# Optimization experiments

Hardware: AMD Instinct MI355X
Metric: run time of the kernel (lower is better)

The kernel has to match this reference:

```python
import jax, jax.numpy as jnp
import numpy as np

N = 65536
APP = 1024
SP = 512
HID = 512
CARD = 16
SUB = HID // CARD  # 32


def setup_inputs() -> dict:
    key = jax.random.key(0)
    ks = jax.random.split(key, 8)
    s1 = 1.0 / np.sqrt(APP)
    s2 = 1.0 / np.sqrt(SP)
    s3 = 1.0 / np.sqrt(SUB)
    return {
        "appearance": jax.random.normal(ks[0], (N, APP), jnp.float32),
        "spatial": jax.random.normal(ks[1], (N, SP), jnp.float32),
        # Batched per-branch weights (torch Linear: y = x @ W.T + b; here stored as [in, out])
        "W1": jax.random.uniform(ks[2], (CARD, APP, SUB), jnp.float32, -s1, s1),
        "b1": jax.random.uniform(ks[3], (CARD, SUB), jnp.float32, -s1, s1),
        "W2": jax.random.uniform(ks[4], (CARD, SP, SUB), jnp.float32, -s2, s2),
        "b2": jax.random.uniform(ks[5], (CARD, SP if False else SUB), jnp.float32, -s2, s2),
        "W3": jax.random.uniform(ks[6], (CARD, SUB, HID), jnp.float32, -s3, s3),
        "b3": jax.random.uniform(ks[7], (CARD, HID), jnp.float32, -s3, s3),
    }


def reference(appearance, spatial, W1, b1, W2, b2, W3, b3):
    # fc1[c] = appearance @ W1[c] + b1[c]; fc2[c] = spatial @ W2[c] + b2[c]
    h1 = jnp.einsum('na,cas->ncs', appearance, W1) + b1[None]  # [N, C, SUB]
    h2 = jnp.einsum('np,cps->ncs', spatial, W2) + b2[None]     # [N, C, SUB]
    h = jax.nn.relu(h1 + h2)
    # sum over branches of (h[:,c] @ W3[c] + b3[c]) == einsum + sum of biases
    out = jnp.einsum('ncs,csh->nh', h, W3) + jnp.sum(b3, axis=0)[None]  # [N, HID]
    return jax.nn.relu(out)
```

## Files before the change

kernel.cpp:

```cpp
#include <hip/hip_runtime.h>
#include <hip/hip_bf16.h>

typedef __attribute__((ext_vector_type(4))) float floatx4;
typedef __attribute__((ext_vector_type(8))) short bf16x8;

__device__ __forceinline__ unsigned short f2bf(float f) {
    union { float f; unsigned u; } v; v.f = f;
    unsigned r = v.u + 0x7fffu + ((v.u >> 16) & 1u);
    return (unsigned short)(r >> 16);
}

__device__ __forceinline__ bf16x8 cvt8(float4 lo, float4 hi) {
    union { __hip_bfloat16 b[8]; bf16x8 v; } u;
    u.b[0] = __float2bfloat16(lo.x); u.b[1] = __float2bfloat16(lo.y);
    u.b[2] = __float2bfloat16(lo.z); u.b[3] = __float2bfloat16(lo.w);
    u.b[4] = __float2bfloat16(hi.x); u.b[5] = __float2bfloat16(hi.y);
    u.b[6] = __float2bfloat16(hi.z); u.b[7] = __float2bfloat16(hi.w);
    return u.v;
}

__device__ __forceinline__ void dma16(const void* gsrc, void* ldst) {
    __builtin_amdgcn_global_load_lds(
        (const __attribute__((address_space(1))) unsigned*)gsrc,
        (__attribute__((address_space(3))) unsigned*)ldst, 16, 0, 0);
}

__global__ void prep_kernel(const float* __restrict__ W1, const float* __restrict__ b1,
                            const float* __restrict__ W2, const float* __restrict__ b2,
                            const float* __restrict__ W3, const float* __restrict__ b3,
                            unsigned short* __restrict__ wcat, unsigned short* __restrict__ w3f,
                            float* __restrict__ bias12, float* __restrict__ bias3s)
{
    int tid = blockIdx.x * 256 + threadIdx.x;
    if (tid < 98304) {
        int l  = tid & 63;
        int nt = (tid >> 6) & 31;
        int kc = tid >> 11;
        int n  = nt * 16 + (l & 15);
        int k0 = kc * 32 + ((l >> 4) << 3);
        int c = n >> 5, s = n & 31;
        union { unsigned short us[8]; int4 v; } pk;
        const float* src = (k0 < 1024) ? (W1 + c * 32768 + k0 * 32 + s)
                                       : (W2 + c * 16384 + (k0 - 1024) * 32 + s);
        #pragma unroll
        for (int j = 0; j < 8; ++j) pk.us[j] = f2bf(src[j * 32]);
        *(int4*)(wcat + (size_t)tid * 8) = pk.v;
    } else if (tid < 131072) {
        int t  = tid - 98304;
        int l  = t & 63;
        int nt = (t >> 6) & 31;
        int kc = t >> 11;
        int n  = nt * 16 + (l & 15);
        int k0 = kc * 32 + ((l >> 4) << 3);
        union { unsigned short us[8]; int4 v; } pk;
        const float* src = W3 + k0 * 512 + n;
        #pragma unroll
        for (int j = 0; j < 8; ++j) pk.us[j] = f2bf(src[j * 512]);
        *(int4*)(w3f + (size_t)t * 8) = pk.v;
    } else if (tid < 131584) {
        int n = tid - 131072;
        bias12[n] = b1[n] + b2[n];
        float sacc = 0.f;
        #pragma unroll
        for (int c = 0; c < 16; ++c) sacc += b3[c * 512 + n];
        bias3s[n] = sacc;
    }
}

__global__ __launch_bounds__(512, 4) void fused_main(
    const float* __restrict__ app, const float* __restrict__ sp,
    const unsigned short* __restrict__ wcat, const unsigned short* __restrict__ w3f,
    const float* __restrict__ bias12, const float* __restrict__ bias3s,
    float* __restrict__ out)
{
    __shared__ union {
        float          As32[3][8][2][64][4];
        unsigned short Hf[4][16][64][8];
    } sh;
    char* shb = (char*)&sh;

    const int tid = (int)threadIdx.x;
    const int w   = tid >> 6;
    const int l   = tid & 63;
    const int rowbase = (int)blockIdx.x * 64;

    const int half = w >> 2, mtw = w & 3;
    const int grow = rowbase + mtw * 16 + (l & 15);
    const char* appB = (const char*)app + (size_t)grow * 4096 + half * 128 + (l >> 4) * 32;
    const char* spB  = (const char*)sp  + (size_t)grow * 2048 + half * 128 + (l >> 4) * 32;

    #define DMA_T(t) do {                                                     \
        const char* _g = ((t) < 16) ? (appB + (t) * 256)                      \
                                    : (spB + ((t) - 16) * 256);               \
        char* _d = shb + ((t) % 3) * 16384 + w * 2048;                        \
        dma16(_g,      _d);                                                   \
        dma16(_g + 16, _d + 1024);                                            \
    } while (0)

    #define BLOAD(kp) do {                                                    \
        const unsigned short* _wp = wbase + (size_t)(kp) * 32768;             \
        _Pragma("unroll")                                                     \
        for (int i = 0; i < 8; ++i)                                           \
            bcur[i] = *(const bf16x8*)(_wp + (i >> 2) * 16384 + (i & 3) * 512);\
    } while (0)

    #define PERIOD_CORE(p) do {                                               \
        const int _bo = ((p) % 3) * 16384;                                    \
        bf16x8 af[4];                                                         \
        _Pragma("unroll")                                                     \
        for (int mt = 0; mt < 4; ++mt) {                                      \
            float4 lo = *(const float4*)(shb + _bo + mt * 2048 + l * 16);     \
            float4 hi = *(const float4*)(shb + _bo + mt * 2048 + 1024 + l * 16);\
            af[mt] = cvt8(lo, hi);                                            \
        }                                                                     \
        __builtin_amdgcn_s_setprio(1);                                        \
        _Pragma("unroll")                                                     \
        for (int mt = 0; mt < 4; ++mt)                                        \
            _Pragma("unroll")                                                 \
            for (int nt = 0; nt < 4; ++nt)                                    \
                acc[mt][nt] = __builtin_amdgcn_mfma_f32_16x16x32_bf16(        \
                    af[mt], bcur[nt], acc[mt][nt], 0, 0, 0);                  \
        __builtin_amdgcn_s_setprio(0);                                        \
        _Pragma("unroll")                                                     \
        for (int mt = 0; mt < 4; ++mt) {                                      \
            float4 lo = *(const float4*)(shb + _bo + (4 + mt) * 2048 + l * 16);\
            float4 hi = *(const float4*)(shb + _bo + (4 + mt) * 2048 + 1024 + l * 16);\
            af[mt] = cvt8(lo, hi);                                            \
        }                                                                     \
        __builtin_amdgcn_s_setprio(1);                                        \
        _Pragma("unroll")                                                     \
        for (int mt = 0; mt < 4; ++mt)                                        \
            _Pragma("unroll")                                                 \
            for (int nt = 0; nt < 4; ++nt)                                    \
                acc[mt][nt] = __builtin_amdgcn_mfma_f32_16x16x32_bf16(        \
                    af[mt], bcur[4 + nt], acc[mt][nt], 0, 0, 0);              \
        __builtin_amdgcn_s_setprio(0);                                        \
    } while (0)

    floatx4 acc[4][4];
    #pragma unroll
    for (int mt = 0; mt < 4; ++mt)
        #pragma unroll
        for (int nt = 0; nt < 4; ++nt)
            acc[mt][nt] = (floatx4){0.f, 0.f, 0.f, 0.f};

    const unsigned short* wbase = wcat + (size_t)w * 2048 + (size_t)l * 8;

    bf16x8 bcur[8];
    BLOAD(0);
    DMA_T(0);
    DMA_T(1);
    asm volatile("s_waitcnt vmcnt(2)" ::: "memory");
    __builtin_amdgcn_s_barrier();
    asm volatile("" ::: "memory");

    for (int p = 0; p < 22; ++p) {
        PERIOD_CORE(p);
        BLOAD(p + 1);
        DMA_T(p + 2);
        asm volatile("s_waitcnt vmcnt(10)" ::: "memory");
        __builtin_amdgcn_s_barrier();
        asm volatile("" ::: "memory");
    }
    PERIOD_CORE(22);
    BLOAD(23);
    asm volatile("s_waitcnt vmcnt(8)" ::: "memory");
    __builtin_amdgcn_s_barrier();
    asm volatile("" ::: "memory");
    PERIOD_CORE(23);
    __builtin_amdgcn_s_barrier();
    asm volatile("" ::: "memory");

    const unsigned short* w3base = w3f + (size_t)w * 2048 + (size_t)l * 8;
    bf16x8 b3[8];
    #pragma unroll
    for (int i = 0; i < 8; ++i)
        b3[i] = *(const bf16x8*)(w3base + (i >> 2) * 16384 + (i & 3) * 512);

    #pragma unroll
    for (int nt = 0; nt < 4; ++nt) {
        const int colg = w * 64 + nt * 16 + (l & 15);
        const float bv = bias12[colg];
        const int kc  = colg >> 5;
        const int lhi = ((colg >> 3) & 3) << 4;
        const int j   = colg & 7;
        #pragma unroll
        for (int mt = 0; mt < 4; ++mt)
            #pragma unroll
            for (int r = 0; r < 4; ++r) {
                const int rlow = ((l >> 4) << 2) + r;
                float v = acc[mt][nt][r] + bv;
                v = fmaxf(v, 0.f);
                sh.Hf[mt][kc][lhi + rlow][j] = f2bf(v);
            }
    }
    asm volatile("s_waitcnt lgkmcnt(0)" ::: "memory");
    __builtin_amdgcn_s_barrier();
    asm volatile("" ::: "memory");

    #pragma unroll
    for (int mt = 0; mt < 4; ++mt)
        #pragma unroll
        for (int nt = 0; nt < 4; ++nt)
            acc[mt][nt] = (floatx4){0.f, 0.f, 0.f, 0.f};

    for (int q = 0; q < 8; ++q) {
        bf16x8 af[4];
        #pragma unroll
        for (int mt = 0; mt < 4; ++mt)
            af[mt] = *(const bf16x8*)(&sh.Hf[mt][2 * q][l][0]);
        __builtin_amdgcn_s_setprio(1);
        #pragma unroll
        for (int mt = 0; mt < 4; ++mt)
            #pragma unroll
            for (int nt = 0; nt < 4; ++nt)
                acc[mt][nt] = __builtin_amdgcn_mfma_f32_16x16x32_bf16(
                    af[mt], b3[nt], acc[mt][nt], 0, 0, 0);
        __builtin_amdgcn_s_setprio(0);
        #pragma unroll
        for (int mt = 0; mt < 4; ++mt)
            af[mt] = *(const bf16x8*)(&sh.Hf[mt][2 * q + 1][l][0]);
        __builtin_amdgcn_s_setprio(1);
        #pragma unroll
        for (int mt = 0; mt < 4; ++mt)
            #pragma unroll
            for (int nt = 0; nt < 4; ++nt)
                acc[mt][nt] = __builtin_amdgcn_mfma_f32_16x16x32_bf16(
                    af[mt], b3[4 + nt], acc[mt][nt], 0, 0, 0);
        __builtin_amdgcn_s_setprio(0);
        if (q + 1 < 8) {
            const unsigned short* wp = w3base + (size_t)(q + 1) * 32768;
            #pragma unroll
            for (int i = 0; i < 8; ++i)
                b3[i] = *(const bf16x8*)(wp + (i >> 2) * 16384 + (i & 3) * 512);
        }
    }

    #pragma unroll
    for (int nt = 0; nt < 4; ++nt) {
        const int colg = w * 64 + nt * 16 + (l & 15);
        const float bv = bias3s[colg];
        #pragma unroll
        for (int mt = 0; mt < 4; ++mt)
            #pragma unroll
            for (int r = 0; r < 4; ++r) {
                const int rowg = mt * 16 + ((l >> 4) << 2) + r;
                float v = acc[mt][nt][r] + bv;
                v = fmaxf(v, 0.f);
                out[(size_t)(rowbase + rowg) * 512 + colg] = v;
            }
    }
    #undef PERIOD_CORE
    #undef BLOAD
    #undef DMA_T
}

extern "C" void kernel_launch(void* const* d_in, const int* in_sizes, int n_in,
                              void* d_out, int out_size, void* d_ws, size_t ws_size,
                              hipStream_t stream)
{
    const float* app = (const float*)d_in[0];
    const float* sp  = (const float*)d_in[1];
    const float* W1  = (const float*)d_in[2];
    const float* b1  = (const float*)d_in[3];
    const float* W2  = (const float*)d_in[4];
    const float* b2  = (const float*)d_in[5];
    const float* W3  = (const float*)d_in[6];
    const float* b3  = (const float*)d_in[7];

    char* ws = (char*)d_ws;
    unsigned short* wcat  = (unsigned short*)(ws);
    unsigned short* w3f   = (unsigned short*)(ws + 1572864);
    float*          b12   = (float*)(ws + 2097152);
    float*          b3s   = (float*)(ws + 2099200);

    prep_kernel<<<514, 256, 0, stream>>>(W1, b1, W2, b2, W3, b3, wcat, w3f, b12, b3s);

    float* outp = (float*)d_out;
    fused_main<<<65536 / 64, 512, 0, stream>>>(app, sp, wcat, w3f, b12, b3s, outp);
}
```

Baseline: 627.1 us.

## Replace LDS-staged triple-buffered A pipeline with direct global loads per wave

Drops the global_load_lds DMA triple-buffer and its per-period barriers for the first GEMM stage. Each wave now loads its A fragments (fp32 appearance/spatial rows) straight from global memory into registers, converts them to bf16, and loads B fragments per 32-wide k chunk. This removes the LDS traffic and barrier synchronisation. In exchange, every wave redundantly reads the same activation rows, about 8x more global/L2 reads of the A operand, and there is no explicit prefetch overlap. The LDS footprint shrinks to only the H buffer, which may raise occupancy.

```diff
diff --git a/kernel.cpp b/kernel.cpp
--- a/kernel.cpp
+++ b/kernel.cpp
@@ -17,12 +17,6 @@
     u.b[4] = __float2bfloat16(hi.x); u.b[5] = __float2bfloat16(hi.y);
     u.b[6] = __float2bfloat16(hi.z); u.b[7] = __float2bfloat16(hi.w);
     return u.v;
-}
-
-__device__ __forceinline__ void dma16(const void* gsrc, void* ldst) {
-    __builtin_amdgcn_global_load_lds(
-        (const __attribute__((address_space(1))) unsigned*)gsrc,
-        (__attribute__((address_space(3))) unsigned*)ldst, 16, 0, 0);
 }
 
 __global__ void prep_kernel(const float* __restrict__ W1, const float* __restrict__ b1,
@@ -73,44 +67,36 @@
     const float* __restrict__ bias12, const float* __restrict__ bias3s,
     float* __restrict__ out)
 {
-    __shared__ union {
-        float          As32[3][8][2][64][4];
-        unsigned short Hf[4][16][64][8];
-    } sh;
-    char* shb = (char*)&sh;
+    __shared__ unsigned short Hf[4][16][64][8];
 
     const int tid = (int)threadIdx.x;
     const int w   = tid >> 6;
     const int l   = tid & 63;
     const int rowbase = (int)blockIdx.x * 64;
 
-    const int half = w >> 2, mtw = w & 3;
-    const int grow = rowbase + mtw * 16 + (l & 15);
-    const char* appB = (const char*)app + (size_t)grow * 4096 + half * 128 + (l >> 4) * 32;
-    const char* spB  = (const char*)sp  + (size_t)grow * 2048 + half * 128 + (l >> 4) * 32;
-
-    #define DMA_T(t) do {                                                     \
-        const char* _g = ((t) < 16) ? (appB + (t) * 256)                      \
-                                    : (spB + ((t) - 16) * 256);               \
-        char* _d = shb + ((t) % 3) * 16384 + w * 2048;                        \
-        dma16(_g,      _d);                                                   \
-        dma16(_g + 16, _d + 1024);                                            \
-    } while (0)
-
-    #define BLOAD(kp) do {                                                    \
-        const unsigned short* _wp = wbase + (size_t)(kp) * 32768;             \
+    const int lm = l & 15;
+    const int lk = (l >> 4) << 3;
+    const float* aF = app + (size_t)(rowbase + lm) * 1024 + lk;
+    const float* sF = sp  + (size_t)(rowbase + lm) * 512  + lk;
+    const unsigned short* wbase = wcat + (size_t)w * 2048 + (size_t)l * 8;
+
+    floatx4 acc[4][4];
+    #pragma unroll
+    for (int mt = 0; mt < 4; ++mt)
+        #pragma unroll
+        for (int nt = 0; nt < 4; ++nt)
+            acc[mt][nt] = (floatx4){0.f, 0.f, 0.f, 0.f};
+
+    #define CHUNK(ASRC, MTSTR, KC) do {                                       \
+        bf16x8 bfr[4];                                                        \
         _Pragma("unroll")                                                     \
-        for (int i = 0; i < 8; ++i)                                           \
-            bcur[i] = *(const bf16x8*)(_wp + (i >> 2) * 16384 + (i & 3) * 512);\
-    } while (0)
-
-    #define PERIOD_CORE(p) do {                                               \
-        const int _bo = ((p) % 3) * 16384;                                    \
+        for (int nt = 0; nt < 4; ++nt)                                        \
+            bfr[nt] = *(const bf16x8*)(wbase + (size_t)(KC) * 16384 + nt * 512);\
         bf16x8 af[4];                                                         \
         _Pragma("unroll")                                                     \
         for (int mt = 0; mt < 4; ++mt) {                                      \
-            float4 lo = *(const float4*)(shb + _bo + mt * 2048 + l * 16);     \
-            float4 hi = *(const float4*)(shb + _bo + mt * 2048 + 1024 + l * 16);\
+            float4 lo = *(const float4*)((ASRC) + mt * (MTSTR));              \
+            float4 hi = *(const float4*)((ASRC) + mt * (MTSTR) + 4);          \
             af[mt] = cvt8(lo, hi);                                            \
         }                                                                     \
         __builtin_amdgcn_s_setprio(1);                                        \
@@ -119,57 +105,14 @@
             _Pragma("unroll")                                                 \
             for (int nt = 0; nt < 4; ++nt)                                    \
                 acc[mt][nt] = __builtin_amdgcn_mfma_f32_16x16x32_bf16(        \
-                    af[mt], bcur[nt], acc[mt][nt], 0, 0, 0);                  \
-        __builtin_amdgcn_s_setprio(0);                                        \
-        _Pragma("unroll")                                                     \
-        for (int mt = 0; mt < 4; ++mt) {                                      \
-            float4 lo = *(const float4*)(shb + _bo + (4 + mt) * 2048 + l * 16);\
-            float4 hi = *(const float4*)(shb + _bo + (4 + mt) * 2048 + 1024 + l * 16);\
-            af[mt] = cvt8(lo, hi);                                            \
-        }                                                                     \
-        __builtin_amdgcn_s_setprio(1);                                        \
-        _Pragma("unroll")                                                     \
-        for (int mt = 0; mt < 4; ++mt)                                        \
-            _Pragma("unroll")                                                 \
-            for (int nt = 0; nt < 4; ++nt)                                    \
-                acc[mt][nt] = __builtin_amdgcn_mfma_f32_16x16x32_bf16(        \
-                    af[mt], bcur[4 + nt], acc[mt][nt], 0, 0, 0);              \
+                    af[mt], bfr[nt], acc[mt][nt], 0, 0, 0);                   \
         __builtin_amdgcn_s_setprio(0);                                        \
     } while (0)
 
-    floatx4 acc[4][4];
-    #pragma unroll
-    for (int mt = 0; mt < 4; ++mt)
-        #pragma unroll
-        for (int nt = 0; nt < 4; ++nt)
-            acc[mt][nt] = (floatx4){0.f, 0.f, 0.f, 0.f};
-
-    const unsigned short* wbase = wcat + (size_t)w * 2048 + (size_t)l * 8;
-
-    bf16x8 bcur[8];
-    BLOAD(0);
-    DMA_T(0);
-    DMA_T(1);
-    asm volatile("s_waitcnt vmcnt(2)" ::: "memory");
-    __builtin_amdgcn_s_barrier();
-    asm volatile("" ::: "memory");
-
-    for (int p = 0; p < 22; ++p) {
-        PERIOD_CORE(p);
-        BLOAD(p + 1);
-        DMA_T(p + 2);
-        asm volatile("s_waitcnt vmcnt(10)" ::: "memory");
-        __builtin_amdgcn_s_barrier();
-        asm volatile("" ::: "memory");
-    }
-    PERIOD_CORE(22);
-    BLOAD(23);
-    asm volatile("s_waitcnt vmcnt(8)" ::: "memory");
-    __builtin_amdgcn_s_barrier();
-    asm volatile("" ::: "memory");
-    PERIOD_CORE(23);
-    __builtin_amdgcn_s_barrier();
-    asm volatile("" ::: "memory");
+    for (int kc = 0; kc < 32; ++kc)
+        CHUNK(aF + kc * 32, 16384, kc);
+    for (int kc = 0; kc < 16; ++kc)
+        CHUNK(sF + kc * 32, 8192, 32 + kc);
 
     const unsigned short* w3base = w3f + (size_t)w * 2048 + (size_t)l * 8;
     bf16x8 b3[8];
@@ -191,7 +134,7 @@
                 const int rlow = ((l >> 4) << 2) + r;
                 float v = acc[mt][nt][r] + bv;
                 v = fmaxf(v, 0.f);
-                sh.Hf[mt][kc][lhi + rlow][j] = f2bf(v);
+                Hf[mt][kc][lhi + rlow][j] = f2bf(v);
             }
     }
     asm volatile("s_waitcnt lgkmcnt(0)" ::: "memory");
@@ -208,7 +151,7 @@
         bf16x8 af[4];
         #pragma unroll
         for (int mt = 0; mt < 4; ++mt)
-            af[mt] = *(const bf16x8*)(&sh.Hf[mt][2 * q][l][0]);
+            af[mt] = *(const bf16x8*)(&Hf[mt][2 * q][l][0]);
         __builtin_amdgcn_s_setprio(1);
         #pragma unroll
         for (int mt = 0; mt < 4; ++mt)
@@ -219,7 +162,7 @@
         __builtin_amdgcn_s_setprio(0);
         #pragma unroll
         for (int mt = 0; mt < 4; ++mt)
-            af[mt] = *(const bf16x8*)(&sh.Hf[mt][2 * q + 1][l][0]);
+            af[mt] = *(const bf16x8*)(&Hf[mt][2 * q + 1][l][0]);
         __builtin_amdgcn_s_setprio(1);
         #pragma unroll
         for (int mt = 0; mt < 4; ++mt)
@@ -250,9 +193,7 @@
                 out[(size_t)(rowbase + rowg) * 512 + colg] = v;
             }
     }
-    #undef PERIOD_CORE
-    #undef BLOAD
-    #undef DMA_T
+    #undef CHUNK
 }
 
 extern "C" void kernel_launch(void* const* d_in, const int* in_sizes, int n_in,
```

New measurement: 801.1 us. 27.8% more time.
